# Performance work log

Measured on AMD Instinct MI355X. Metric: run time of the kernel, lower is better.

## Reference

```python
import jax, jax.numpy as jnp
import numpy as np

G, A = 512, 24            # graphs, atoms per graph (constant -> static edge count)
N, E = G * A, G * A * A   # nodes, fully-connected edges per graph (incl. self loops)
HID, TDIM, BB, NFREQ, NLAYER = 128, 256, 64, 10, 4
DIS = NFREQ * 2 * 3                     # SinusoidsEmbedding dim = 60
EDGE_IN = 2 * HID + 6 + DIS             # 322
LAT_IN = HID + 16 + TDIM                # 400


def setup_inputs() -> dict:
    key = jax.random.key(0)
    ks = jax.random.split(key, 32)
    s = 0.02

    # block-diagonal fully-connected edge list (dense_to_sparse of ones(A,A) per graph)
    local = np.arange(A)
    off = np.repeat(np.arange(G) * A, A * A)
    e0 = np.tile(np.repeat(local, A), G) + off   # row index
    e1 = np.tile(np.tile(local, A), G) + off     # col index
    edge_index = jnp.asarray(np.stack([e0, e1]), dtype=jnp.int32)

    inp = {
        "t": jax.random.normal(ks[0], (G, TDIM), jnp.float32),
        "bb_embs": jax.random.normal(ks[1], (N, BB), jnp.float32),
        "frac_coords": jax.random.uniform(ks[2], (N, 3), jnp.float32),
        "so3_vecs": jax.random.normal(ks[3], (N, 16), jnp.float32),
        "lattices": jax.random.normal(ks[4], (G, 6), jnp.float32),
        "num_atoms": jnp.full((G,), A, dtype=jnp.int32),
        "node2graph": jnp.repeat(jnp.arange(G, dtype=jnp.int32), A),
        "edge_index": edge_index,
        # parameters
        "W_emb": jax.random.normal(ks[5], (BB, HID)) * s,
        "b_emb": jnp.zeros((HID,), jnp.float32),
        "W_lat": jax.random.normal(ks[6], (LAT_IN, HID)) * s,
        "b_lat": jnp.zeros((HID,), jnp.float32),
        "We1": jax.random.normal(ks[7], (NLAYER, EDGE_IN, HID)) * s,
        "be1": jnp.zeros((NLAYER, HID), jnp.float32),
        "We2": jax.random.normal(ks[8], (NLAYER, HID, HID)) * s,
        "be2": jnp.zeros((NLAYER, HID), jnp.float32),
        "Wn1": jax.random.normal(ks[9], (NLAYER, 2 * HID, HID)) * s,
        "bn1": jnp.zeros((NLAYER, HID), jnp.float32),
        "Wn2": jax.random.normal(ks[10], (NLAYER, HID, HID)) * s,
        "bn2": jnp.zeros((NLAYER, HID), jnp.float32),
        "W_coord": jax.random.normal(ks[11], (HID, 3)) * s,
        "W_lattice": jax.random.normal(ks[12], (HID, 6)) * s,
        "W_so3": jax.random.normal(ks[13], (HID, 4)) * s,
    }
    return inp


def reference(t, bb_embs, frac_coords, so3_vecs, lattices, num_atoms, node2graph,
              edge_index, W_emb, b_emb, W_lat, b_lat,
              We1, be1, We2, be2, Wn1, bn1, Wn2, bn2,
              W_coord, W_lattice, W_so3):
    n_nodes = bb_embs.shape[0]
    n_graphs = t.shape[0]
    e0, e1 = edge_index[0], edge_index[1]

    # gen_edges (period == 1): frac_diff = (x_j - x_i) % 1
    frac_diff = jnp.mod(frac_coords[e1] - frac_coords[e0], 1.0)
    # SinusoidsEmbedding (detached in torch)
    freqs = 2.0 * jnp.pi * jnp.arange(NFREQ, dtype=frac_diff.dtype)
    ang = (frac_diff[:, :, None] * freqs).reshape(-1, 3 * NFREQ)   # [E, 30]
    pe = jax.lax.stop_gradient(jnp.concatenate([jnp.sin(ang), jnp.cos(ang)], -1))  # [E, 60]

    edge2graph = node2graph[e0]
    lat_e = lattices[edge2graph]                                   # [E, 6]

    # node embedding + latent projection (no activation on atom_latent_emb)
    h0 = jnp.concatenate([bb_embs @ W_emb + b_emb, so3_vecs, t[node2graph]], axis=1)
    h = h0 @ W_lat + b_lat                                          # [N, HID]

    counts = jax.ops.segment_sum(jnp.ones((e0.shape[0], 1), h.dtype), e0,
                                 num_segments=n_nodes)
    counts = jnp.maximum(counts, 1.0)

    def csp_layer(h, p):
        we1, b1, we2, b2, wn1, c1, wn2, c2 = p
        ein = jnp.concatenate([h[e0], h[e1], lat_e, pe], axis=1)    # [E, 322]
        ef = jax.nn.silu(jax.nn.silu(ein @ we1 + b1) @ we2 + b2)    # [E, HID]
        agg = jax.ops.segment_sum(ef, e0, num_segments=n_nodes) / counts  # mean
        nin = jnp.concatenate([h, agg], axis=1)                     # [N, 2*HID]
        out = jax.nn.silu(jax.nn.silu(nin @ wn1 + c1) @ wn2 + c2)
        return h + out, None

    h, _ = jax.lax.scan(csp_layer, h, (We1, be1, We2, be2, Wn1, bn1, Wn2, bn2))

    coord_out = h @ W_coord                                          # [N, 3]
    so3_out = h @ W_so3
    so3_out = so3_out / jnp.linalg.norm(so3_out, axis=-1, keepdims=True)

    gcounts = jax.ops.segment_sum(jnp.ones((n_nodes, 1), h.dtype), node2graph,
                                  num_segments=n_graphs)
    gfeat = jax.ops.segment_sum(h, node2graph, num_segments=n_graphs) / gcounts
    lattice_out = gfeat @ W_lattice                                  # [G, 6]

    # back2interval (period == 1) applied to coord_out + frac_coords
    return (lattice_out, jnp.mod(coord_out + frac_coords, 1.0), so3_out)
```

## Files before the change

### kernel.cpp

```cpp
#include <hip/hip_runtime.h>
#include <hip/hip_bf16.h>


#define NG 512
#define NA 24
#define HID 128
#define TDIM 256
#define NBB 64
#define TPB 256
#define LFRAGS 208
#define OFF_A 0
#define OFF_B 32
#define OFF_D 64
#define OFF_E2 80
#define OFF_N1 112
#define OFF_N2 176
#define FRAG_BYTES (832ull * 1024ull)
#define TL_BYTES   (512ull * 128ull * 4ull)
#define PE_BYTES   (512ull * 6ull * 12ull * 512ull * 2ull)

typedef __bf16 bf16x8 __attribute__((ext_vector_type(8)));
typedef float  f32x4  __attribute__((ext_vector_type(4)));

#define O_HB   0
#define O_BAUG 6528
#define O_AGG  14720
#define O_MID  21248
#define O_TL   47360
#define O_FRAC 47872
#define O_LAT6 48160
#define SMEM_BYTES 48192

__device__ __forceinline__ float silu_f(float x) {
    return x * __builtin_amdgcn_rcpf(1.0f + __expf(-x));
}

__device__ __forceinline__ unsigned short cvtbf(float x) {
    __hip_bfloat16 b = __float2bfloat16(x);
    return *reinterpret_cast<unsigned short*>(&b);
}

__device__ __forceinline__ unsigned pk2(float a, float b) {
    unsigned ua = __builtin_bit_cast(unsigned, a) + 0x8000u;
    unsigned ub = __builtin_bit_cast(unsigned, b) + 0x8000u;
    return __builtin_amdgcn_perm(ub, ua, 0x07060302u);
}

__device__ __forceinline__ f32x4 MFMA(bf16x8 a, bf16x8 b, f32x4 c) {
    return __builtin_amdgcn_mfma_f32_16x16x32_bf16(a, b, c, 0, 0, 0);
}

__device__ __forceinline__ bf16x8 gfrag(const unsigned short* ws, int fragIdx, int l) {
    const int4* p = reinterpret_cast<const int4*>(ws + (size_t)fragIdx * 512) + l;
    return __builtin_bit_cast(bf16x8, *p);
}
__device__ __forceinline__ bf16x8 lfrag(const unsigned short* buf, int stride, int row0, int kofs, int l) {
    const int4* p = reinterpret_cast<const int4*>(buf + (row0 + (l & 15)) * stride + kofs + ((l >> 4) << 3));
    return __builtin_bit_cast(bf16x8, *p);
}
__device__ __forceinline__ bf16x8 lfragRaw(const unsigned short* buf, int fragIdx, int l) {
    const int4* p = reinterpret_cast<const int4*>(buf + fragIdx * 512) + l;
    return __builtin_bit_cast(bf16x8, *p);
}
__device__ __forceinline__ bf16x8 augfrag(int row, int q) {
    int i0l = row / 24;
    int ja  = row - i0l * 24;
    int k2  = 4 + ja;
    bf16x8 v;
#pragma unroll
    for (int e = 0; e < 8; ++e) {
        int k = q * 8 + e;
        bool one = (k == i0l) || (k == k2) || (k == 28);
        v[e] = one ? (__bf16)1.0f : (__bf16)0.0f;
    }
    return v;
}

__device__ __forceinline__ float pe_val(int gI, int e, const float* fd) {
    int d, trig, f; bool valid = true;
    if (gI < 6) { d = gI % 3; trig = gI / 3; f = e; }
    else if (gI == 6) {
        const int dt[8] = {0,0,1,1,2,2,0,0};
        const int tt[8] = {0,0,0,0,0,0,1,1};
        d = dt[e]; trig = tt[e]; f = 8 + (e & 1);
    } else {
        if (e < 4) { const int dt[4] = {1,1,2,2}; d = dt[e]; trig = 1; f = 8 + (e & 1); }
        else { valid = false; d = 0; trig = 0; f = 0; }
    }
    if (!valid) return 0.f;
    return __builtin_amdgcn_sinf(fd[d] * (float)f + 0.25f * (float)trig);
}

#define FMA4(ACC, S, W) { (ACC).x += (S)*(W).x; (ACC).y += (S)*(W).y; \
                          (ACC).z += (S)*(W).z; (ACC).w += (S)*(W).w; }

__device__ __forceinline__ float4 ld4(const float* __restrict__ p) {
    return *reinterpret_cast<const float4*>(p);
}

__global__ void __launch_bounds__(TPB) pack_weights(
    const float* __restrict__ We1, const float* __restrict__ We2,
    const float* __restrict__ Wn1, const float* __restrict__ Wn2,
    const float* __restrict__ t_in, const float* __restrict__ W_lat,
    unsigned short* __restrict__ ws, float* __restrict__ tlAll, int useTl)
{
    if (blockIdx.x >= 208) {
        if (!useTl) return;
        int b2 = blockIdx.x - 208;
        int gl = threadIdx.x >> 5, lane32 = threadIdx.x & 31;
        int g = b2 * 8 + gl, c0 = lane32 * 4;
        float4 acc = make_float4(0.f, 0.f, 0.f, 0.f);
        const float* tg = t_in + (size_t)g * TDIM;
#pragma unroll 4
        for (int k = 0; k < TDIM; ++k) {
            float tv = tg[k];
            float4 w = ld4(W_lat + (size_t)(144 + k) * HID + c0);
            FMA4(acc, tv, w);
        }
        *reinterpret_cast<float4*>(tlAll + (size_t)g * HID + c0) = acc;
        return;
    }
    int w = blockIdx.x * 4 + (threadIdx.x >> 6);
    int l = threadIdx.x & 63;
    int q = l >> 4, c16 = l & 15;
    int layer = w / LFRAGS, r = w % LFRAGS;
    const float* src; int K4, seg, klim; bool isPE = false;
    if (r < 32)       { seg = 0;   K4 = 4; src = We1 + (size_t)layer*322*128;           klim = 128; }
    else if (r < 64)  { seg = 32;  K4 = 4; src = We1 + (size_t)layer*322*128 + 128*128; klim = 128; }
    else if (r < 80)  { seg = 64;  K4 = 2; src = We1 + (size_t)layer*322*128 + 262*128; klim = 64; isPE = true; }
    else if (r < 112) { seg = 80;  K4 = 4; src = We2 + (size_t)layer*128*128;           klim = 128; }
    else if (r < 176) { seg = 112; K4 = 8; src = Wn1 + (size_t)layer*256*128;           klim = 256; }
    else              { seg = 176; K4 = 4; src = Wn2 + (size_t)layer*128*128;           klim = 128; }
    int rr = r - seg; int nt = rr / K4, ks = rr % K4;
    unsigned short vals[8];
#pragma unroll
    for (int j = 0; j < 8; ++j) {
        int row = ks * 32 + q * 8 + j;
        float v = 0.f;
        if (row < klim) {
            if (isPE) {
                int gI = row >> 3, e = row & 7;
                int d = 0, trig = 0, f = 0; bool valid = true;
                if (gI < 6) { d = gI % 3; trig = gI / 3; f = e; }
                else if (gI == 6) {
                    const int dt[8] = {0,0,1,1,2,2,0,0};
                    const int tt[8] = {0,0,0,0,0,0,1,1};
                    d = dt[e]; trig = tt[e]; f = 8 + (e & 1);
                } else {
                    if (e < 4) { const int dt[4] = {1,1,2,2};
                                 d = dt[e]; trig = 1; f = 8 + (e & 1); }
                    else valid = false;
                }
                if (valid) v = src[(size_t)(trig * 30 + d * 10 + f) * 128 + nt * 16 + c16];
            } else {
                v = src[(size_t)row * 128 + nt * 16 + c16];
            }
        }
        vals[j] = cvtbf(v);
    }
    unsigned int d0 = (unsigned)vals[0] | ((unsigned)vals[1] << 16);
    unsigned int d1 = (unsigned)vals[2] | ((unsigned)vals[3] << 16);
    unsigned int d2 = (unsigned)vals[4] | ((unsigned)vals[5] << 16);
    unsigned int d3 = (unsigned)vals[6] | ((unsigned)vals[7] << 16);
    int4 o = make_int4((int)d0, (int)d1, (int)d2, (int)d3);
    *reinterpret_cast<int4*>(ws + ((size_t)w * 64 + l) * 8) = o;
}

__global__ void __launch_bounds__(TPB) gen_pe(
    const float* __restrict__ frac, unsigned short* __restrict__ peT)
{
    const int g = blockIdx.x;
    __shared__ float fracS[NA * 3];
    if (threadIdx.x < NA * 3) fracS[threadIdx.x] = frac[(size_t)g * NA * 3 + threadIdx.x];
    __syncthreads();
    for (int s = threadIdx.x; s < 6 * 12 * 64; s += TPB) {
        int l = s & 63;
        int sf = s >> 6;
        int fragIdx = sf % 12, ck = sf / 12;
        int rt = fragIdx >> 1, ks = fragIdx & 1;
        int r = rt * 16 + (l & 15);
        int q = l >> 4;
        int gI = ks * 4 + q;
        int i0l = r / 24, j = r - i0l * 24;
        int i0 = ck * 4 + i0l;
        float fd[3];
#pragma unroll
        for (int d = 0; d < 3; ++d) fd[d] = fracS[j * 3 + d] - fracS[i0 * 3 + d];
        unsigned p[4];
#pragma unroll
        for (int ep = 0; ep < 4; ++ep)
            p[ep] = pk2(pe_val(gI, 2 * ep, fd), pe_val(gI, 2 * ep + 1, fd));
        *reinterpret_cast<int4*>(peT + (((size_t)(g * 6 + ck) * 12 + fragIdx) * 512 + l * 8)) =
            make_int4(p[0], p[1], p[2], p[3]);
    }
}

template<int USEPE>
__global__ void __launch_bounds__(TPB, 2) cspnet_mfma(
    const float* __restrict__ t_in, const float* __restrict__ bb_embs,
    const float* __restrict__ frac, const float* __restrict__ so3,
    const float* __restrict__ lattices,
    const float* __restrict__ W_emb, const float* __restrict__ b_emb,
    const float* __restrict__ W_lat, const float* __restrict__ b_lat,
    const float* __restrict__ We1, const float* __restrict__ be1,
    const float* __restrict__ be2, const float* __restrict__ bn1,
    const float* __restrict__ bn2,
    const float* __restrict__ W_coord, const float* __restrict__ W_lattice,
    const float* __restrict__ W_so3,
    const unsigned short* __restrict__ wsU, const float* __restrict__ tlAll,
    const unsigned short* __restrict__ peT,
    int useTl, float* __restrict__ out)
{
    __shared__ __align__(16) char smem[SMEM_BYTES];
    unsigned short* hbU   = (unsigned short*)(smem + O_HB);
    unsigned short* baugU = (unsigned short*)(smem + O_BAUG);
    unsigned short* aggU  = (unsigned short*)(smem + O_AGG);
    unsigned short* midU  = (unsigned short*)(smem + O_MID);
    unsigned short* t1U   = midU;
    float* tlS   = (float*)(smem + O_TL);
    float* fracS = (float*)(smem + O_FRAC);
    float* lat6S = (float*)(smem + O_LAT6);
    float* embS  = (float*)(smem + O_MID);
    float* hscrF = (float*)(smem + O_MID + 12288);

    const int g   = blockIdx.x;
    const int tid = threadIdx.x;
    const int l   = tid & 63;
    const int wv  = tid >> 6;
    const int q   = l >> 4;
    const int c16 = l & 15;
    const int mh  = wv >> 1;
    const float inv24 = 1.0f / 24.0f;
    const f32x4 FZ = {0.f, 0.f, 0.f, 0.f};

    if (tid < NA * 3) {
        int i = tid / 3, d = tid - i * 3;
        fracS[i * 3 + d] = frac[(size_t)(g * NA + i) * 3 + d];
    }
    if (tid < 6) lat6S[tid] = lattices[(size_t)g * 6 + tid];
    for (int v = tid; v < 384; v += TPB) {
        int ct = v / 48, rest = v % 48, cl = rest / 3, jp = 5 + rest % 3;
        baugU[ct * 512 + (48 + cl) * 8 + jp] = 0;
    }
    if (useTl) {
        if (tid < HID) tlS[tid] = tlAll[(size_t)g * HID + tid];
    } else if (tid < HID) {
        float acc = 0.f;
        const float* tg = t_in + (size_t)g * TDIM;
        for (int k = 0; k < TDIM; ++k)
            acc += tg[k] * W_lat[(size_t)(144 + k) * HID + tid];
        tlS[tid] = acc;
    }

    {
        const int cg = tid & 31, rg = tid >> 5, c0 = cg * 4;
        float4 acc[3];
        float4 be = ld4(b_emb + c0);
        acc[0] = be; acc[1] = be; acc[2] = be;
        const float* bbg = bb_embs + (size_t)(g * NA) * NBB;
#pragma unroll 4
        for (int k = 0; k < NBB; ++k) {
            float4 w = ld4(W_emb + (size_t)k * HID + c0);
            float b0v = bbg[rg * NBB + k];
            float b1v = bbg[(rg + 8) * NBB + k];
            float b2v = bbg[(rg + 16) * NBB + k];
            FMA4(acc[0], b0v, w); FMA4(acc[1], b1v, w); FMA4(acc[2], b2v, w);
        }
#pragma unroll
        for (int s = 0; s < 3; ++s)
            *reinterpret_cast<float4*>(&embS[(rg + 8 * s) * HID + c0]) = acc[s];
    }
    __syncthreads();

    {
        const int cg = tid & 31, rg = tid >> 5, c0 = cg * 4;
        float4 acc[3];
        float4 bl = ld4(b_lat + c0);
        float4 tv = *reinterpret_cast<const float4*>(tlS + c0);
        bl.x += tv.x; bl.y += tv.y; bl.z += tv.z; bl.w += tv.w;
        acc[0] = bl; acc[1] = bl; acc[2] = bl;
#pragma unroll 4
        for (int k = 0; k < HID; ++k) {
            float4 w = ld4(W_lat + (size_t)k * HID + c0);
            float e0 = embS[rg * HID + k], e1 = embS[(rg + 8) * HID + k], e2 = embS[(rg + 16) * HID + k];
            FMA4(acc[0], e0, w); FMA4(acc[1], e1, w); FMA4(acc[2], e2, w);
        }
        const float* so3g = so3 + (size_t)(g * NA) * 16;
#pragma unroll
        for (int k = 0; k < 16; ++k) {
            float4 w = ld4(W_lat + (size_t)(HID + k) * HID + c0);
            float s0 = so3g[rg * 16 + k], s1 = so3g[(rg + 8) * 16 + k], s2 = so3g[(rg + 16) * 16 + k];
            FMA4(acc[0], s0, w); FMA4(acc[1], s1, w); FMA4(acc[2], s2, w);
        }
#pragma unroll
        for (int s = 0; s < 3; ++s) {
            int row = rg + 8 * s;
            *reinterpret_cast<float4*>(&hscrF[row * HID + c0]) = acc[s];
            uint2 pv = make_uint2(pk2(acc[s].x, acc[s].y), pk2(acc[s].z, acc[s].w));
            *reinterpret_cast<uint2*>(&hbU[row * 136 + c0]) = pv;
        }
    }
    __syncthreads();

    float hreg[2][2][4];
#pragma unroll
    for (int ctl = 0; ctl < 2; ++ctl)
#pragma unroll
        for (int rt = 0; rt < 2; ++rt) {
            int row = rt * 16 + c16;
#pragma unroll
            for (int r = 0; r < 4; ++r)
                hreg[ctl][rt][r] = (row < 24) ? hscrF[row * HID + (wv * 2 + ctl) * 16 + q * 4 + r] : 0.f;
        }
    __syncthreads();

    bf16x8 augB[3];
#pragma unroll
    for (int rtl = 0; rtl < 3; ++rtl)
        augB[rtl] = augfrag((mh * 3 + rtl) * 16 + c16, q);

    for (int ly = 0; ly < 4; ++ly) {
        const int LOFF = ly * LFRAGS;
        const float* be1_l = be1 + ly * HID;
        const float* We1_l = We1 + (size_t)ly * 322 * HID;
        const float* be2_l = be2 + ly * HID;
        const float* bn1_l = bn1 + ly * HID;
        const float* bn2_l = bn2 + ly * HID;

        bf16x8 w1dr[4][2];
#pragma unroll
        for (int ctl = 0; ctl < 4; ++ctl)
#pragma unroll
            for (int ks = 0; ks < 2; ++ks)
                w1dr[ctl][ks] = gfrag(wsU, LOFF + OFF_D + ((wv & 1) * 4 + ctl) * 2 + ks, l);
        float be2r[4];
#pragma unroll
        for (int ntl = 0; ntl < 4; ++ntl)
            be2r[ntl] = be2_l[((wv & 1) * 4 + ntl) * 16 + c16];

        {
            f32x4 pacc[2][2];
#pragma unroll
            for (int a = 0; a < 2; ++a) { pacc[a][0] = FZ; pacc[a][1] = FZ; }
#pragma unroll
            for (int ks = 0; ks < 4; ++ks) {
                bf16x8 b0 = lfrag(hbU, 136, 0, ks * 32, l);
                bf16x8 b1 = lfrag(hbU, 136, 16, ks * 32, l);
#pragma unroll
                for (int ctl = 0; ctl < 2; ++ctl) {
                    bf16x8 a = gfrag(wsU, LOFF + OFF_B + (wv * 2 + ctl) * 4 + ks, l);
                    pacc[ctl][0] = MFMA(a, b0, pacc[ctl][0]);
                    pacc[ctl][1] = MFMA(a, b1, pacc[ctl][1]);
                }
            }
#pragma unroll
            for (int ctl = 0; ctl < 2; ++ctl)
#pragma unroll
                for (int rt = 0; rt < 2; ++rt) {
                    int row = rt * 16 + c16;
                    if (row < 24) {
                        int ka = 4 + row, qp = ka >> 3, jp = ka & 7;
#pragma unroll
                        for (int r = 0; r < 4; ++r) {
                            int c = (wv * 2 + ctl) * 16 + q * 4 + r;
                            baugU[(c >> 4) * 512 + (qp * 16 + (c & 15)) * 8 + jp] = cvtbf(pacc[ctl][rt][r]);
                        }
                    }
                }
        }
        if (tid < HID) {
            float a = be1_l[tid];
#pragma unroll
            for (int k = 0; k < 6; ++k)
                a += lat6S[k] * We1_l[(size_t)(256 + k) * HID + tid];
            int c = tid;
            baugU[(c >> 4) * 512 + (48 + (c & 15)) * 8 + 4] = cvtbf(a);
        }
        __syncthreads();

        for (int ck = 0; ck < 6; ++ck) {
            bf16x8 peF[3][2];
            if constexpr (USEPE) {
                const unsigned short* peG = peT + (size_t)(g * 6 + ck) * 12 * 512;
#pragma unroll
                for (int rtl = 0; rtl < 3; ++rtl) {
                    int rt = mh * 3 + rtl;
                    peF[rtl][0] = lfragRaw(peG, rt * 2, l);
                    peF[rtl][1] = lfragRaw(peG, rt * 2 + 1, l);
                }
            } else {
#pragma unroll
                for (int rtl = 0; rtl < 3; ++rtl) {
                    int r = (mh * 3 + rtl) * 16 + c16;
                    int i0l = (r * 43) >> 10;
                    int j = r - i0l * 24;
                    int i0 = ck * 4 + i0l;
                    float fd[3];
#pragma unroll
                    for (int d = 0; d < 3; ++d)
                        fd[d] = fracS[j * 3 + d] - fracS[i0 * 3 + d];
#pragma unroll
                    for (int ks = 0; ks < 2; ++ks) {
                        int gI = ks * 4 + q;
                        unsigned p[4];
#pragma unroll
                        for (int ep = 0; ep < 4; ++ep)
                            p[ep] = pk2(pe_val(gI, 2 * ep, fd), pe_val(gI, 2 * ep + 1, fd));
                        peF[rtl][ks] = __builtin_bit_cast(bf16x8, make_int4(p[0], p[1], p[2], p[3]));
                    }
                }
            }

            {
                f32x4 hacc[2] = {FZ, FZ};
#pragma unroll
                for (int ks = 0; ks < 4; ++ks) {
                    bf16x8 b = lfrag(hbU, 136, ck * 4, ks * 32, l);
#pragma unroll
                    for (int ctl = 0; ctl < 2; ++ctl) {
                        bf16x8 a = gfrag(wsU, LOFF + OFF_A + (wv * 2 + ctl) * 4 + ks, l);
                        hacc[ctl] = MFMA(a, b, hacc[ctl]);
                    }
                }
                if (c16 < 4) {
#pragma unroll
                    for (int ctl = 0; ctl < 2; ++ctl)
#pragma unroll
                        for (int r = 0; r < 4; ++r) {
                            int c = (wv * 2 + ctl) * 16 + q * 4 + r;
                            baugU[(c >> 4) * 512 + (c & 15) * 8 + c16] = cvtbf(hacc[ctl][r]);
                        }
                }
            }
            __syncthreads();

            {
                const int ct0 = (wv & 1) * 4;
                f32x4 macc[4][3];
#pragma unroll
                for (int a = 0; a < 4; ++a)
#pragma unroll
                    for (int b = 0; b < 3; ++b) macc[a][b] = FZ;
#pragma unroll
                for (int ks = 0; ks < 2; ++ks)
#pragma unroll
                    for (int ctl = 0; ctl < 4; ++ctl)
#pragma unroll
                        for (int rtl = 0; rtl < 3; ++rtl)
                            macc[ctl][rtl] = MFMA(w1dr[ctl][ks], peF[rtl][ks], macc[ctl][rtl]);
#pragma unroll
                for (int ctl = 0; ctl < 4; ++ctl) {
                    bf16x8 a2 = lfragRaw(baugU, ct0 + ctl, l);
#pragma unroll
                    for (int rtl = 0; rtl < 3; ++rtl)
                        macc[ctl][rtl] = MFMA(a2, augB[rtl], macc[ctl][rtl]);
                }
#pragma unroll
                for (int ctl = 0; ctl < 4; ++ctl)
#pragma unroll
                    for (int rtl = 0; rtl < 3; ++rtl) {
                        int row = (mh * 3 + rtl) * 16 + c16;
                        int cb = (ct0 + ctl) * 16 + q * 4;
                        uint2 pv = make_uint2(pk2(silu_f(macc[ctl][rtl][0]), silu_f(macc[ctl][rtl][1])),
                                              pk2(silu_f(macc[ctl][rtl][2]), silu_f(macc[ctl][rtl][3])));
                        *reinterpret_cast<uint2*>(&midU[row * 136 + cb]) = pv;
                    }
            }
            __syncthreads();

            {
                f32x4 eacc[3][4];
#pragma unroll
                for (int a = 0; a < 3; ++a)
#pragma unroll
                    for (int b = 0; b < 4; ++b) eacc[a][b] = FZ;
#pragma unroll
                for (int ks = 0; ks < 4; ++ks) {
                    bf16x8 wb[4];
#pragma unroll
                    for (int ntl = 0; ntl < 4; ++ntl)
                        wb[ntl] = gfrag(wsU, LOFF + OFF_E2 + ((wv & 1) * 4 + ntl) * 4 + ks, l);
                    bf16x8 am[3];
#pragma unroll
                    for (int mtl = 0; mtl < 3; ++mtl)
                        am[mtl] = lfrag(midU, 136, (3 * mh + mtl) * 16, ks * 32, l);
#pragma unroll
                    for (int ntl = 0; ntl < 4; ++ntl)
#pragma unroll
                        for (int mtl = 0; mtl < 3; ++mtl)
                            eacc[mtl][ntl] = MFMA(am[mtl], wb[ntl], eacc[mtl][ntl]);
                }
#pragma unroll
                for (int ntl = 0; ntl < 4; ++ntl) {
                    float s0 = 0.f, s1 = 0.f;
#pragma unroll
                    for (int r = 0; r < 4; ++r) {
                        float e0 = silu_f(eacc[0][ntl][r] + be2r[ntl]);
                        float e1 = silu_f(eacc[1][ntl][r] + be2r[ntl]);
                        float e2 = silu_f(eacc[2][ntl][r] + be2r[ntl]);
                        s0 += e0; s1 += e2;
                        if (q < 2) s0 += e1; else s1 += e1;
                    }
                    s0 += __shfl_xor(s0, 16, 64); s0 += __shfl_xor(s0, 32, 64);
                    s1 += __shfl_xor(s1, 16, 64); s1 += __shfl_xor(s1, 32, 64);
                    if (q == 0) {
                        int i0a = ck * 4 + 2 * mh;
                        int cc = ((wv & 1) * 4 + ntl) * 16 + c16;
                        aggU[i0a * 136 + cc]       = cvtbf(s0 * inv24);
                        aggU[(i0a + 1) * 136 + cc] = cvtbf(s1 * inv24);
                    }
                }
            }
            __syncthreads();
        }

        {
            f32x4 t1a[2][2];
#pragma unroll
            for (int a = 0; a < 2; ++a) { t1a[a][0] = FZ; t1a[a][1] = FZ; }
#pragma unroll
            for (int ks = 0; ks < 8; ++ks) {
                bf16x8 b0, b1;
                if (ks < 4) { b0 = lfrag(hbU, 136, 0, ks * 32, l);  b1 = lfrag(hbU, 136, 16, ks * 32, l); }
                else        { b0 = lfrag(aggU, 136, 0, (ks - 4) * 32, l); b1 = lfrag(aggU, 136, 16, (ks - 4) * 32, l); }
#pragma unroll
                for (int ctl = 0; ctl < 2; ++ctl) {
                    bf16x8 a = gfrag(wsU, LOFF + OFF_N1 + (wv * 2 + ctl) * 8 + ks, l);
                    t1a[ctl][0] = MFMA(a, b0, t1a[ctl][0]);
                    t1a[ctl][1] = MFMA(a, b1, t1a[ctl][1]);
                }
            }
            float bn1r[2][4];
#pragma unroll
            for (int ctl = 0; ctl < 2; ++ctl)
#pragma unroll
                for (int r = 0; r < 4; ++r)
                    bn1r[ctl][r] = bn1_l[(wv * 2 + ctl) * 16 + q * 4 + r];
#pragma unroll
            for (int ctl = 0; ctl < 2; ++ctl)
#pragma unroll
                for (int rt = 0; rt < 2; ++rt) {
                    int row = rt * 16 + c16;
                    int cb = (wv * 2 + ctl) * 16 + q * 4;
                    uint2 pv = make_uint2(pk2(silu_f(t1a[ctl][rt][0] + bn1r[ctl][0]),
                                              silu_f(t1a[ctl][rt][1] + bn1r[ctl][1])),
                                          pk2(silu_f(t1a[ctl][rt][2] + bn1r[ctl][2]),
                                              silu_f(t1a[ctl][rt][3] + bn1r[ctl][3])));
                    *reinterpret_cast<uint2*>(&t1U[row * 136 + cb]) = pv;
                }
        }
        __syncthreads();
        {
            f32x4 t2a[2][2];
#pragma unroll
            for (int a = 0; a < 2; ++a) { t2a[a][0] = FZ; t2a[a][1] = FZ; }
#pragma unroll
            for (int ks = 0; ks < 4; ++ks) {
                bf16x8 b0 = lfrag(t1U, 136, 0, ks * 32, l);
                bf16x8 b1 = lfrag(t1U, 136, 16, ks * 32, l);
#pragma unroll
                for (int ctl = 0; ctl < 2; ++ctl) {
                    bf16x8 a = gfrag(wsU, LOFF + OFF_N2 + (wv * 2 + ctl) * 4 + ks, l);
                    t2a[ctl][0] = MFMA(a, b0, t2a[ctl][0]);
                    t2a[ctl][1] = MFMA(a, b1, t2a[ctl][1]);
                }
            }
            float bn2r[2][4];
#pragma unroll
            for (int ctl = 0; ctl < 2; ++ctl)
#pragma unroll
                for (int r = 0; r < 4; ++r)
                    bn2r[ctl][r] = bn2_l[(wv * 2 + ctl) * 16 + q * 4 + r];
#pragma unroll
            for (int ctl = 0; ctl < 2; ++ctl)
#pragma unroll
                for (int rt = 0; rt < 2; ++rt) {
                    int row = rt * 16 + c16;
#pragma unroll
                    for (int r = 0; r < 4; ++r)
                        hreg[ctl][rt][r] += silu_f(t2a[ctl][rt][r] + bn2r[ctl][r]);
                    if (row < 24) {
                        int cb = (wv * 2 + ctl) * 16 + q * 4;
                        uint2 pv = make_uint2(pk2(hreg[ctl][rt][0], hreg[ctl][rt][1]),
                                              pk2(hreg[ctl][rt][2], hreg[ctl][rt][3]));
                        *reinterpret_cast<uint2*>(&hbU[row * 136 + cb]) = pv;
                    }
                }
        }
        __syncthreads();
    }

#pragma unroll
    for (int ctl = 0; ctl < 2; ++ctl)
#pragma unroll
        for (int rt = 0; rt < 2; ++rt) {
            int row = rt * 16 + c16;
            if (row < 24) {
                float4 v = make_float4(hreg[ctl][rt][0], hreg[ctl][rt][1], hreg[ctl][rt][2], hreg[ctl][rt][3]);
                *reinterpret_cast<float4*>(&hscrF[row * HID + (wv * 2 + ctl) * 16 + q * 4]) = v;
            }
        }
    __syncthreads();

    if (tid < HID) {
        float s = 0.f;
#pragma unroll 4
        for (int i = 0; i < NA; ++i) s += hscrF[i * HID + tid];
        tlS[tid] = s * inv24;
    }
    if (tid < NA * 3) {
        int i = tid / 3, d = tid - i * 3;
        float acc = 0.f;
#pragma unroll 4
        for (int k = 0; k < HID; ++k) acc += hscrF[i * HID + k] * W_coord[k * 3 + d];
        acc += fracS[i * 3 + d];
        acc -= floorf(acc);
        out[(size_t)NG * 6 + (size_t)(g * NA + i) * 3 + d] = acc;
    }
    if (tid < NA) {
        int i = tid;
        float v0 = 0.f, v1 = 0.f, v2 = 0.f, v3 = 0.f;
#pragma unroll 4
        for (int k = 0; k < HID; ++k) {
            float hv = hscrF[i * HID + k];
            v0 += hv * W_so3[k * 4 + 0]; v1 += hv * W_so3[k * 4 + 1];
            v2 += hv * W_so3[k * 4 + 2]; v3 += hv * W_so3[k * 4 + 3];
        }
        float inv = 1.0f / sqrtf(v0 * v0 + v1 * v1 + v2 * v2 + v3 * v3);
        size_t o = (size_t)NG * 6 + (size_t)NG * NA * 3 + (size_t)(g * NA + i) * 4;
        out[o + 0] = v0 * inv; out[o + 1] = v1 * inv;
        out[o + 2] = v2 * inv; out[o + 3] = v3 * inv;
    }
    __syncthreads();
    if (tid < 6) {
        float acc = 0.f;
#pragma unroll 4
        for (int c = 0; c < HID; ++c) acc += tlS[c] * W_lattice[c * 6 + tid];
        out[(size_t)g * 6 + tid] = acc;
    }
}

extern "C" void kernel_launch(void* const* d_in, const int* in_sizes, int n_in,
                              void* d_out, int out_size, void* d_ws, size_t ws_size,
                              hipStream_t stream) {
    const float* t_in    = (const float*)d_in[0];
    const float* bb      = (const float*)d_in[1];
    const float* frac    = (const float*)d_in[2];
    const float* so3     = (const float*)d_in[3];
    const float* lat     = (const float*)d_in[4];
    const float* W_emb   = (const float*)d_in[8];
    const float* b_emb   = (const float*)d_in[9];
    const float* W_lat   = (const float*)d_in[10];
    const float* b_lat   = (const float*)d_in[11];
    const float* We1     = (const float*)d_in[12];
    const float* be1     = (const float*)d_in[13];
    const float* We2     = (const float*)d_in[14];
    const float* be2     = (const float*)d_in[15];
    const float* Wn1     = (const float*)d_in[16];
    const float* bn1     = (const float*)d_in[17];
    const float* Wn2     = (const float*)d_in[18];
    const float* bn2     = (const float*)d_in[19];
    const float* W_coord = (const float*)d_in[20];
    const float* W_latt  = (const float*)d_in[21];
    const float* W_so3   = (const float*)d_in[22];

    unsigned short* ws = (unsigned short*)d_ws;
    float* tlAll = (float*)((char*)d_ws + FRAG_BYTES);
    unsigned short* peT = (unsigned short*)((char*)d_ws + FRAG_BYTES + TL_BYTES);
    int useTl = (ws_size >= FRAG_BYTES + TL_BYTES) ? 1 : 0;
    int usePe = (ws_size >= FRAG_BYTES + TL_BYTES + PE_BYTES) ? 1 : 0;

    hipLaunchKernelGGL(pack_weights, dim3(272), dim3(TPB), 0, stream,
                       We1, We2, Wn1, Wn2, t_in, W_lat, ws, tlAll, useTl);
    if (usePe) {
        hipLaunchKernelGGL(gen_pe, dim3(NG), dim3(TPB), 0, stream, frac, peT);
        hipLaunchKernelGGL(cspnet_mfma<1>, dim3(NG), dim3(TPB), 0, stream,
                           t_in, bb, frac, so3, lat, W_emb, b_emb, W_lat, b_lat,
                           We1, be1, be2, bn1, bn2, W_coord, W_latt, W_so3,
                           (const unsigned short*)ws, (const float*)tlAll,
                           (const unsigned short*)peT, useTl, (float*)d_out);
    } else {
        hipLaunchKernelGGL(cspnet_mfma<0>, dim3(NG), dim3(TPB), 0, stream,
                           t_in, bb, frac, so3, lat, W_emb, b_emb, W_lat, b_lat,
                           We1, be1, be2, bn1, bn2, W_coord, W_latt, W_so3,
                           (const unsigned short*)ws, (const float*)tlAll,
                           (const unsigned short*)peT, useTl, (float*)d_out);
    }
}
```

Before: 322.9 us.

## Precompute per-node h·We1 projections once per layer, remove per-chunk sync

The per-source-node projection (h[e0] @ W_A) is now computed for all 24 nodes once per layer, next to the destination projection, and both go into a widened 64-row augmented K buffer in shared memory. Each edge chunk then selects its rows with a one-hot augmentation fragment spanning two K slices. This removes the per-chunk MFMA pass, the store into shared memory and one __syncthreads from each of the six chunks per layer. In exchange, shared memory grows by about 8 KB and each chunk issues twice as many augmentation MFMAs, plus it rebuilds the one-hot fragments in registers every chunk.

Measured after the change: 330.0 us. +2.2%, slower.

```diff
diff --git a/kernel.cpp b/kernel.cpp
--- a/kernel.cpp
+++ b/kernel.cpp
@@ -24,12 +24,12 @@
 
 #define O_HB   0
 #define O_BAUG 6528
-#define O_AGG  14720
-#define O_MID  21248
-#define O_TL   47360
-#define O_FRAC 47872
-#define O_LAT6 48160
-#define SMEM_BYTES 48192
+#define O_AGG  22912
+#define O_MID  29440
+#define O_TL   55552
+#define O_FRAC 56064
+#define O_LAT6 56352
+#define SMEM_BYTES 56384
 
 __device__ __forceinline__ float silu_f(float x) {
     return x * __builtin_amdgcn_rcpf(1.0f + __expf(-x));
@@ -62,18 +62,10 @@
     const int4* p = reinterpret_cast<const int4*>(buf + fragIdx * 512) + l;
     return __builtin_bit_cast(bf16x8, *p);
 }
-__device__ __forceinline__ bf16x8 augfrag(int row, int q) {
-    int i0l = row / 24;
-    int ja  = row - i0l * 24;
-    int k2  = 4 + ja;
-    bf16x8 v;
-#pragma unroll
-    for (int e = 0; e < 8; ++e) {
-        int k = q * 8 + e;
-        bool one = (k == i0l) || (k == k2) || (k == 28);
-        v[e] = one ? (__bf16)1.0f : (__bf16)0.0f;
-    }
-    return v;
+
+__device__ __forceinline__ int baug_off(int ct, int ka, int col) {
+    int kr = ka & 31;
+    return ct * 1024 + ((ka >> 5) * 512) + ((((kr >> 3) * 16) + col) << 3) + (kr & 7);
 }
 
 __device__ __forceinline__ float pe_val(int gI, int e, const float* fd) {
@@ -238,9 +230,10 @@
         fracS[i * 3 + d] = frac[(size_t)(g * NA + i) * 3 + d];
     }
     if (tid < 6) lat6S[tid] = lattices[(size_t)g * 6 + tid];
-    for (int v = tid; v < 384; v += TPB) {
-        int ct = v / 48, rest = v % 48, cl = rest / 3, jp = 5 + rest % 3;
-        baugU[ct * 512 + (48 + cl) * 8 + jp] = 0;
+    for (int v = tid; v < 1920; v += TPB) {
+        int ct = v / 240; int rest = v - ct * 240;
+        int row = 49 + (rest >> 4); int col = rest & 15;
+        baugU[baug_off(ct, row, col)] = 0;
     }
     if (useTl) {
         if (tid < HID) tlS[tid] = tlAll[(size_t)g * HID + tid];
@@ -314,10 +307,23 @@
         }
     __syncthreads();
 
-    bf16x8 augB[3];
-#pragma unroll
-    for (int rtl = 0; rtl < 3; ++rtl)
-        augB[rtl] = augfrag((mh * 3 + rtl) * 16 + c16, q);
+    int i0lR[3], jR[3];
+#pragma unroll
+    for (int rtl = 0; rtl < 3; ++rtl) {
+        int r = (mh * 3 + rtl) * 16 + c16;
+        i0lR[rtl] = (r * 43) >> 10;
+        jR[rtl]   = r - i0lR[rtl] * 24;
+    }
+    bf16x8 augB1[3];
+#pragma unroll
+    for (int rtl = 0; rtl < 3; ++rtl) {
+        int k2 = 24 + jR[rtl];
+#pragma unroll
+        for (int e = 0; e < 8; ++e) {
+            int k = 32 + q * 8 + e;
+            augB1[rtl][e] = (k == k2 || k == 48) ? (__bf16)1.0f : (__bf16)0.0f;
+        }
+    }
 
     for (int ly = 0; ly < 4; ++ly) {
         const int LOFF = ly * LFRAGS;
@@ -339,18 +345,23 @@
             be2r[ntl] = be2_l[((wv & 1) * 4 + ntl) * 16 + c16];
 
         {
-            f32x4 pacc[2][2];
-#pragma unroll
-            for (int a = 0; a < 2; ++a) { pacc[a][0] = FZ; pacc[a][1] = FZ; }
+            f32x4 pa[2][2], pb[2][2];
+#pragma unroll
+            for (int a = 0; a < 2; ++a) {
+                pa[a][0] = FZ; pa[a][1] = FZ; pb[a][0] = FZ; pb[a][1] = FZ;
+            }
 #pragma unroll
             for (int ks = 0; ks < 4; ++ks) {
                 bf16x8 b0 = lfrag(hbU, 136, 0, ks * 32, l);
                 bf16x8 b1 = lfrag(hbU, 136, 16, ks * 32, l);
 #pragma unroll
                 for (int ctl = 0; ctl < 2; ++ctl) {
-                    bf16x8 a = gfrag(wsU, LOFF + OFF_B + (wv * 2 + ctl) * 4 + ks, l);
-                    pacc[ctl][0] = MFMA(a, b0, pacc[ctl][0]);
-                    pacc[ctl][1] = MFMA(a, b1, pacc[ctl][1]);
+                    bf16x8 aA = gfrag(wsU, LOFF + OFF_A + (wv * 2 + ctl) * 4 + ks, l);
+                    bf16x8 aB = gfrag(wsU, LOFF + OFF_B + (wv * 2 + ctl) * 4 + ks, l);
+                    pa[ctl][0] = MFMA(aA, b0, pa[ctl][0]);
+                    pa[ctl][1] = MFMA(aA, b1, pa[ctl][1]);
+                    pb[ctl][0] = MFMA(aB, b0, pb[ctl][0]);
+                    pb[ctl][1] = MFMA(aB, b1, pb[ctl][1]);
                 }
             }
 #pragma unroll
@@ -359,11 +370,12 @@
                 for (int rt = 0; rt < 2; ++rt) {
                     int row = rt * 16 + c16;
                     if (row < 24) {
-                        int ka = 4 + row, qp = ka >> 3, jp = ka & 7;
 #pragma unroll
                         for (int r = 0; r < 4; ++r) {
                             int c = (wv * 2 + ctl) * 16 + q * 4 + r;
-                            baugU[(c >> 4) * 512 + (qp * 16 + (c & 15)) * 8 + jp] = cvtbf(pacc[ctl][rt][r]);
+                            int ctI = c >> 4, col = c & 15;
+                            baugU[baug_off(ctI, row, col)]      = cvtbf(pa[ctl][rt][r]);
+                            baugU[baug_off(ctI, 24 + row, col)] = cvtbf(pb[ctl][rt][r]);
                         }
                     }
                 }
@@ -373,74 +385,66 @@
 #pragma unroll
             for (int k = 0; k < 6; ++k)
                 a += lat6S[k] * We1_l[(size_t)(256 + k) * HID + tid];
-            int c = tid;
-            baugU[(c >> 4) * 512 + (48 + (c & 15)) * 8 + 4] = cvtbf(a);
+            baugU[baug_off(tid >> 4, 48, tid & 15)] = cvtbf(a);
         }
         __syncthreads();
 
         for (int ck = 0; ck < 6; ++ck) {
-            bf16x8 peF[3][2];
-            if constexpr (USEPE) {
-                const unsigned short* peG = peT + (size_t)(g * 6 + ck) * 12 * 512;
-#pragma unroll
-                for (int rtl = 0; rtl < 3; ++rtl) {
-                    int rt = mh * 3 + rtl;
-                    peF[rtl][0] = lfragRaw(peG, rt * 2, l);
-                    peF[rtl][1] = lfragRaw(peG, rt * 2 + 1, l);
-                }
-            } else {
-#pragma unroll
-                for (int rtl = 0; rtl < 3; ++rtl) {
-                    int r = (mh * 3 + rtl) * 16 + c16;
-                    int i0l = (r * 43) >> 10;
-                    int j = r - i0l * 24;
-                    int i0 = ck * 4 + i0l;
-                    float fd[3];
-#pragma unroll
-                    for (int d = 0; d < 3; ++d)
-                        fd[d] = fracS[j * 3 + d] - fracS[i0 * 3 + d];
-#pragma unroll
-                    for (int ks = 0; ks < 2; ++ks) {
-                        int gI = ks * 4 + q;
-                        unsigned p[4];
-#pragma unroll
-                        for (int ep = 0; ep < 4; ++ep)
-                            p[ep] = pk2(pe_val(gI, 2 * ep, fd), pe_val(gI, 2 * ep + 1, fd));
-                        peF[rtl][ks] = __builtin_bit_cast(bf16x8, make_int4(p[0], p[1], p[2], p[3]));
-                    }
-                }
-            }
-
-            {
-                f32x4 hacc[2] = {FZ, FZ};
-#pragma unroll
-                for (int ks = 0; ks < 4; ++ks) {
-                    bf16x8 b = lfrag(hbU, 136, ck * 4, ks * 32, l);
-#pragma unroll
-                    for (int ctl = 0; ctl < 2; ++ctl) {
-                        bf16x8 a = gfrag(wsU, LOFF + OFF_A + (wv * 2 + ctl) * 4 + ks, l);
-                        hacc[ctl] = MFMA(a, b, hacc[ctl]);
-                    }
-                }
-                if (c16 < 4) {
-#pragma unroll
-                    for (int ctl = 0; ctl < 2; ++ctl)
-#pragma unroll
-                        for (int r = 0; r < 4; ++r) {
-                            int c = (wv * 2 + ctl) * 16 + q * 4 + r;
-                            baugU[(c >> 4) * 512 + (c & 15) * 8 + c16] = cvtbf(hacc[ctl][r]);
-                        }
-                }
-            }
-            __syncthreads();
-
             {
                 const int ct0 = (wv & 1) * 4;
+                bf16x8 peF[3][2];
+                if constexpr (USEPE) {
+                    const unsigned short* peG = peT + (size_t)(g * 6 + ck) * 12 * 512;
+#pragma unroll
+                    for (int rtl = 0; rtl < 3; ++rtl) {
+                        peF[rtl][0] = lfragRaw(peG, (mh * 3 + rtl) * 2, l);
+                        peF[rtl][1] = lfragRaw(peG, (mh * 3 + rtl) * 2 + 1, l);
+                    }
+                } else {
+#pragma unroll
+                    for (int rtl = 0; rtl < 3; ++rtl) {
+                        int i0 = ck * 4 + i0lR[rtl];
+                        float fd[3];
+#pragma unroll
+                        for (int d = 0; d < 3; ++d)
+                            fd[d] = fracS[jR[rtl] * 3 + d] - fracS[i0 * 3 + d];
+#pragma unroll
+                        for (int ks = 0; ks < 2; ++ks) {
+                            int gI = ks * 4 + q;
+                            unsigned p[4];
+#pragma unroll
+                            for (int ep = 0; ep < 4; ++ep)
+                                p[ep] = pk2(pe_val(gI, 2 * ep, fd), pe_val(gI, 2 * ep + 1, fd));
+                            peF[rtl][ks] = __builtin_bit_cast(bf16x8, make_int4(p[0], p[1], p[2], p[3]));
+                        }
+                    }
+                }
+                bf16x8 aug0[3];
+#pragma unroll
+                for (int rtl = 0; rtl < 3; ++rtl) {
+                    int k1 = ck * 4 + i0lR[rtl];
+                    int k2 = 24 + jR[rtl];
+#pragma unroll
+                    for (int e = 0; e < 8; ++e) {
+                        int k = q * 8 + e;
+                        aug0[rtl][e] = (k == k1 || k == k2) ? (__bf16)1.0f : (__bf16)0.0f;
+                    }
+                }
                 f32x4 macc[4][3];
 #pragma unroll
                 for (int a = 0; a < 4; ++a)
 #pragma unroll
                     for (int b = 0; b < 3; ++b) macc[a][b] = FZ;
+#pragma unroll
+                for (int ctl = 0; ctl < 4; ++ctl) {
+                    bf16x8 a20 = lfragRaw(baugU, (ct0 + ctl) * 2, l);
+                    bf16x8 a21 = lfragRaw(baugU, (ct0 + ctl) * 2 + 1, l);
+#pragma unroll
+                    for (int rtl = 0; rtl < 3; ++rtl) {
+                        macc[ctl][rtl] = MFMA(a20, aug0[rtl], macc[ctl][rtl]);
+                        macc[ctl][rtl] = MFMA(a21, augB1[rtl], macc[ctl][rtl]);
+                    }
+                }
 #pragma unroll
                 for (int ks = 0; ks < 2; ++ks)
 #pragma unroll
@@ -448,13 +452,6 @@
 #pragma unroll
                         for (int rtl = 0; rtl < 3; ++rtl)
                             macc[ctl][rtl] = MFMA(w1dr[ctl][ks], peF[rtl][ks], macc[ctl][rtl]);
-#pragma unroll
-                for (int ctl = 0; ctl < 4; ++ctl) {
-                    bf16x8 a2 = lfragRaw(baugU, ct0 + ctl, l);
-#pragma unroll
-                    for (int rtl = 0; rtl < 3; ++rtl)
-                        macc[ctl][rtl] = MFMA(a2, augB[rtl], macc[ctl][rtl]);
-                }
 #pragma unroll
                 for (int ctl = 0; ctl < 4; ++ctl)
 #pragma unroll
```
